# Kernel optimization log

Hardware: AMD Instinct MI355X
Metric: run time of the kernel (lower is better)

Reference implementation:

```python
import jax, jax.numpy as jnp
import numpy as np

H = 4          # number of heads
C = 32         # head dim (H*C == D)
INF = 1e9
EPS = 1e-5


def setup_inputs() -> dict:
    key = jax.random.key(0)
    ks = jax.random.split(key, 8)
    B, N, D = 1, 256, 128
    x = jax.random.normal(ks[0], (B, N, N, D), dtype=jnp.float32)
    mask = jnp.ones((B, N, N), dtype=jnp.float32)
    s = 1.0 / np.sqrt(D)
    return {
        "x": x,
        "mask": mask,
        "ln_w": jnp.ones((D,), jnp.float32),
        "ln_b": jnp.zeros((D,), jnp.float32),
        "w_tri": jax.random.normal(ks[1], (D, H), jnp.float32) * s,
        "w_q": jax.random.normal(ks[2], (D, H * C), jnp.float32) * s,
        "w_k": jax.random.normal(ks[3], (D, H * C), jnp.float32) * s,
        "w_v": jax.random.normal(ks[4], (D, H * C), jnp.float32) * s,
        "w_g": jax.random.normal(ks[5], (D, H * C), jnp.float32) * s,
        "b_g": jnp.ones((H * C,), jnp.float32),
        "w_o": jax.random.normal(ks[6], (H * C, D), jnp.float32) * s,
        "b_o": jnp.zeros((D,), jnp.float32),
    }


def reference(x, mask, ln_w, ln_b, w_tri, w_q, w_k, w_v, w_g, b_g, w_o, b_o):
    B, I, J, D = x.shape
    # LayerNorm over channel dim
    mu = jnp.mean(x, axis=-1, keepdims=True)
    var = jnp.mean(jnp.square(x - mu), axis=-1, keepdims=True)
    xn = (x - mu) * jax.lax.rsqrt(var + EPS) * ln_w + ln_b

    # Triangle bias: linear D->H, permute_final_dims((2,0,1)) -> [B,H,I,J], unsqueeze(-4) -> [B,1,H,I,J]
    tri_bias = jnp.einsum("bijd,dh->bhij", xn, w_tri)[:, None]
    # Mask bias: inf*(mask[...,:,None,None,:]-1) -> [B,I,1,1,J]
    mask_bias = INF * (mask[:, :, None, None, :] - 1.0)

    # Gated MHA per row I, attending across columns J
    q = (xn @ w_q).reshape(B, I, J, H, C) * (1.0 / np.sqrt(C))
    k = (xn @ w_k).reshape(B, I, J, H, C)
    v = (xn @ w_v).reshape(B, I, J, H, C)
    scores = jnp.einsum("bimhc,binhc->bihmn", q, k) + tri_bias + mask_bias
    attn = jax.nn.softmax(scores, axis=-1)
    o = jnp.einsum("bihmn,binhc->bimhc", attn, v)
    g = jax.nn.sigmoid((xn @ w_g + b_g).reshape(B, I, J, H, C))
    o = (g * o).reshape(B, I, J, H * C)
    return o @ w_o + b_o
```

## Files before the change

### kernel.cpp

```cpp
#include <hip/hip_runtime.h>
#include <hip/hip_bf16.h>

#define INF_F 1e9f
#define EPS_F 1e-5f
#define QSCALE 0.1767766952966369f
#define SM_SHIFT 16.0f

typedef __attribute__((ext_vector_type(8))) short short8;
typedef __attribute__((ext_vector_type(4))) float f32x4;

__device__ __forceinline__ unsigned short f2bf(float f) {
    union { float f; unsigned int u; } v; v.f = f;
    unsigned int r = v.u + 0x7FFFu + ((v.u >> 16) & 1u);
    return (unsigned short)(r >> 16);
}
__device__ __forceinline__ float bf2f(unsigned short b) {
    union { unsigned int u; float f; } v; v.u = ((unsigned int)b) << 16; return v.f;
}
__device__ __forceinline__ unsigned int pack2bf(float a, float b) {
    return (unsigned int)f2bf(a) | ((unsigned int)f2bf(b) << 16);
}

__global__ __launch_bounds__(256) void prep_weights(
    const float* __restrict__ wq, const float* __restrict__ wk,
    const float* __restrict__ wv, const float* __restrict__ wg,
    const float* __restrict__ wo, unsigned short* __restrict__ wt)
{
    const int m = blockIdx.x;
    const float* W = (m == 0) ? wq : (m == 1) ? wk : (m == 2) ? wv : (m == 3) ? wg : wo;
    const float scale = (m == 0) ? QSCALE : 1.0f;
    unsigned short* out = wt + m * 16384;
    const int t = threadIdx.x;
    #pragma unroll
    for (int j = 0; j < 8; ++j) {
        int o = t * 64 + j * 8;
        int n = o >> 7, k0 = o & 127;
        short8 v;
        #pragma unroll
        for (int jj = 0; jj < 8; ++jj)
            v[jj] = (short)f2bf(W[(size_t)(k0 + jj) * 128 + n] * scale);
        *reinterpret_cast<short8*>(out + o) = v;
    }
}

__global__ __launch_bounds__(512, 4) void ln_proj_kernel(
    const float* __restrict__ x, const float* __restrict__ ln_w, const float* __restrict__ ln_b,
    const float* __restrict__ w_tri, const unsigned short* __restrict__ wt,
    const float* __restrict__ b_g,
    unsigned short* __restrict__ qb, unsigned short* __restrict__ kb,
    unsigned short* __restrict__ vb, unsigned short* __restrict__ gb,
    float* __restrict__ tri_bias)
{
    __shared__ unsigned short xs[128][136];
    __shared__ unsigned short wb[128][136];
    __shared__ float wt_s[512];
    __shared__ float bgs[128];

    const int tid = threadIdx.x;
    const int p0  = blockIdx.x * 128;

    if (tid < 128) bgs[tid] = b_g[tid];
    wt_s[tid] = w_tri[tid];

    {
        const int c4 = (tid & 31) * 4;
        const float4 lw = *reinterpret_cast<const float4*>(ln_w + c4);
        const float4 lb = *reinterpret_cast<const float4*>(ln_b + c4);
        #pragma unroll
        for (int r = 0; r < 8; ++r) {
            int idx = r * 512 + tid;
            int px  = idx >> 5;
            float4 v = *reinterpret_cast<const float4*>(x + (size_t)(p0 + px) * 128 + c4);
            float s  = v.x + v.y + v.z + v.w;
            float ss = v.x * v.x + v.y * v.y + v.z * v.z + v.w * v.w;
            #pragma unroll
            for (int mk = 1; mk <= 16; mk <<= 1) {
                s  += __shfl_xor(s, mk);
                ss += __shfl_xor(ss, mk);
            }
            float mu   = s * 0.0078125f;
            float rstd = rsqrtf(ss * 0.0078125f - mu * mu + EPS_F);
            float a0 = (v.x - mu) * rstd * lw.x + lb.x;
            float a1 = (v.y - mu) * rstd * lw.y + lb.y;
            float a2 = (v.z - mu) * rstd * lw.z + lb.z;
            float a3 = (v.w - mu) * rstd * lw.w + lb.w;
            *reinterpret_cast<unsigned int*>(&xs[px][c4])     = pack2bf(a0, a1);
            *reinterpret_cast<unsigned int*>(&xs[px][c4 + 2]) = pack2bf(a2, a3);
        }
    }
    __syncthreads();

    {
        const int px = tid >> 2, hh = tid & 3;
        float acc = 0.f;
        #pragma unroll
        for (int kq = 0; kq < 128; kq += 8) {
            short8 xv = *reinterpret_cast<const short8*>(&xs[px][kq]);
            #pragma unroll
            for (int j = 0; j < 8; ++j)
                acc = fmaf(bf2f((unsigned short)xv[j]), wt_s[(kq + j) * 4 + hh], acc);
        }
        tri_bias[hh * 65536 + p0 + px] = acc;
    }

    const int lane = tid & 63, wid = tid >> 6;
    const int lrow = lane & 15, lgrp = lane >> 4;
    const int m0 = (wid >> 1) * 32, n0 = (wid & 1) * 64;

    for (int y = 0; y < 4; ++y) {
        __syncthreads();
        const unsigned short* Wsrc = wt + y * 16384;
        #pragma unroll
        for (int r = 0; r < 4; ++r) {
            int idx = r * 512 + tid;
            int n = idx >> 4, k8 = (idx & 15) * 8;
            *reinterpret_cast<short8*>(&wb[n][k8]) =
                *reinterpret_cast<const short8*>(Wsrc + n * 128 + k8);
        }
        __syncthreads();

        f32x4 acc[2][4];
        #pragma unroll
        for (int mt = 0; mt < 2; ++mt)
            #pragma unroll
            for (int nt = 0; nt < 4; ++nt) acc[mt][nt] = f32x4{0.f, 0.f, 0.f, 0.f};

        #pragma unroll
        for (int kk = 0; kk < 4; ++kk) {
            short8 af[2], bfr[4];
            #pragma unroll
            for (int mt = 0; mt < 2; ++mt)
                af[mt] = *reinterpret_cast<const short8*>(&xs[m0 + mt * 16 + lrow][kk * 32 + lgrp * 8]);
            #pragma unroll
            for (int nt = 0; nt < 4; ++nt)
                bfr[nt] = *reinterpret_cast<const short8*>(&wb[n0 + nt * 16 + lrow][kk * 32 + lgrp * 8]);
            #pragma unroll
            for (int mt = 0; mt < 2; ++mt)
                #pragma unroll
                for (int nt = 0; nt < 4; ++nt)
                    acc[mt][nt] = __builtin_amdgcn_mfma_f32_16x16x32_bf16(af[mt], bfr[nt], acc[mt][nt], 0, 0, 0);
        }
        __syncthreads();

        #pragma unroll
        for (int mt = 0; mt < 2; ++mt)
            #pragma unroll
            for (int nt = 0; nt < 4; ++nt)
                #pragma unroll
                for (int r = 0; r < 4; ++r) {
                    int row = m0 + mt * 16 + lgrp * 4 + r;
                    int col = n0 + nt * 16 + lrow;
                    float v = acc[mt][nt][r];
                    if (y == 3) v = 1.f / (1.f + __expf(-(v + bgs[col])));
                    wb[row][col] = f2bf(v);
                }
        __syncthreads();

        unsigned short* outp = (y == 0) ? qb : (y == 1) ? kb : (y == 2) ? vb : gb;
        #pragma unroll
        for (int r = 0; r < 4; ++r) {
            int idx = r * 512 + tid;
            int px = idx >> 4, c8 = (idx & 15) * 8;
            *reinterpret_cast<short8*>(outp + (size_t)(p0 + px) * 128 + c8) =
                *reinterpret_cast<const short8*>(&wb[px][c8]);
        }
    }
}

__global__ __launch_bounds__(512, 4) void attn_kernel(
    const unsigned short* qbuf, const unsigned short* __restrict__ kbuf,
    const unsigned short* __restrict__ vbuf, const unsigned short* __restrict__ gbuf,
    const float* __restrict__ tri_bias, const float* __restrict__ mask,
    unsigned short* og)
{
    __shared__ unsigned short Ks[256][40];
    __shared__ unsigned short Vt[32][264];
    __shared__ float maskb[256];

    const int tid = threadIdx.x;
    const int i  = blockIdx.x;
    const int h  = blockIdx.y >> 1;
    const int rg = blockIdx.y & 1;
    const size_t base = (size_t)i * 32768 + (size_t)h * 32;

    #pragma unroll
    for (int r = 0; r < 2; ++r) {
        int idx = r * 512 + tid;
        int n = idx >> 2, c8 = (idx & 3) * 8;
        short8 kv = *reinterpret_cast<const short8*>(kbuf + base + (size_t)n * 128 + c8);
        short8 vv = *reinterpret_cast<const short8*>(vbuf + base + (size_t)n * 128 + c8);
        *reinterpret_cast<short8*>(&Ks[n][c8]) = kv;
        #pragma unroll
        for (int j = 0; j < 8; ++j) {
            int row = c8 + j;
            Vt[row][n ^ (((row >> 3) & 3) << 3)] = (unsigned short)vv[j];
        }
    }
    if (tid < 256) maskb[tid] = INF_F * (mask[i * 256 + tid] - 1.0f);
    __syncthreads();

    const int lane = tid & 63;
    const int wid  = tid >> 6;
    const int q    = lane & 15;
    const int g    = lane >> 4;
    const int q0   = rg * 128 + wid * 16;

    short8 qf = *reinterpret_cast<const short8*>(qbuf + base + (size_t)(q0 + q) * 128 + g * 8);

    const float* biasrow = tri_bias + (size_t)h * 65536 + (size_t)(q0 + q) * 256;
    const f32x4 z = {0.f, 0.f, 0.f, 0.f};
    f32x4 oacc[2] = {z, z};
    float lsum = 0.f;
    const int xr0 = (((q >> 3) & 1) << 3);
    const int xr1 = ((((16 + q) >> 3) & 3) << 3);

    #pragma unroll
    for (int ch = 0; ch < 8; ++ch) {
        const int nb = ch * 32;
        short8 kf0 = *reinterpret_cast<const short8*>(&Ks[nb + q][g * 8]);
        short8 kf1 = *reinterpret_cast<const short8*>(&Ks[nb + 16 + q][g * 8]);
        f32x4 s0 = __builtin_amdgcn_mfma_f32_16x16x32_bf16(kf0, qf, z, 0, 0, 0);
        f32x4 s1 = __builtin_amdgcn_mfma_f32_16x16x32_bf16(kf1, qf, z, 0, 0, 0);
        f32x4 bv0 = *reinterpret_cast<const f32x4*>(biasrow + nb + g * 4);
        f32x4 bv1 = *reinterpret_cast<const f32x4*>(biasrow + nb + 16 + g * 4);
        f32x4 mv0 = *reinterpret_cast<const f32x4*>(&maskb[nb + g * 4]);
        f32x4 mv1 = *reinterpret_cast<const f32x4*>(&maskb[nb + 16 + g * 4]);
        s0 += bv0 + mv0;
        s1 += bv1 + mv1;
        float p00 = __expf(s0[0] - SM_SHIFT), p01 = __expf(s0[1] - SM_SHIFT);
        float p02 = __expf(s0[2] - SM_SHIFT), p03 = __expf(s0[3] - SM_SHIFT);
        float p10 = __expf(s1[0] - SM_SHIFT), p11 = __expf(s1[1] - SM_SHIFT);
        float p12 = __expf(s1[2] - SM_SHIFT), p13 = __expf(s1[3] - SM_SHIFT);
        lsum += ((p00 + p01) + (p02 + p03)) + ((p10 + p11) + (p12 + p13));
        unsigned int A0 = pack2bf(p00, p01), A1 = pack2bf(p02, p03);
        unsigned int B0 = pack2bf(p10, p11), B1 = pack2bf(p12, p13);
        unsigned int A16_0 = (unsigned int)__shfl_xor((int)A0, 16);
        unsigned int A16_1 = (unsigned int)__shfl_xor((int)A1, 16);
        unsigned int B16_0 = (unsigned int)__shfl_xor((int)B0, 16);
        unsigned int B16_1 = (unsigned int)__shfl_xor((int)B1, 16);
        unsigned int A32_0 = (unsigned int)__shfl_xor((int)A0, 32);
        unsigned int A32_1 = (unsigned int)__shfl_xor((int)A1, 32);
        unsigned int B32_0 = (unsigned int)__shfl_xor((int)B0, 32);
        unsigned int B32_1 = (unsigned int)__shfl_xor((int)B1, 32);
        unsigned int A48_0 = (unsigned int)__shfl_xor((int)A16_0, 32);
        unsigned int A48_1 = (unsigned int)__shfl_xor((int)A16_1, 32);
        unsigned int B48_0 = (unsigned int)__shfl_xor((int)B16_0, 32);
        unsigned int B48_1 = (unsigned int)__shfl_xor((int)B16_1, 32);
        union { unsigned int u[4]; short8 s; } pu;
        pu.u[0] = (g == 0) ? A0    : (g == 1) ? A48_0 : (g == 2) ? B32_0 : B16_0;
        pu.u[1] = (g == 0) ? A1    : (g == 1) ? A48_1 : (g == 2) ? B32_1 : B16_1;
        pu.u[2] = (g == 0) ? A16_0 : (g == 1) ? A32_0 : (g == 2) ? B48_0 : B0;
        pu.u[3] = (g == 0) ? A16_1 : (g == 1) ? A32_1 : (g == 2) ? B48_1 : B1;
        short8 vf0 = *reinterpret_cast<const short8*>(&Vt[q][(nb + g * 8) ^ xr0]);
        short8 vf1 = *reinterpret_cast<const short8*>(&Vt[16 + q][(nb + g * 8) ^ xr1]);
        oacc[0] = __builtin_amdgcn_mfma_f32_16x16x32_bf16(pu.s, vf0, oacc[0], 0, 0, 0);
        oacc[1] = __builtin_amdgcn_mfma_f32_16x16x32_bf16(pu.s, vf1, oacc[1], 0, 0, 0);
    }

    lsum += __shfl_xor(lsum, 16);
    lsum += __shfl_xor(lsum, 32);

    float linv = 1.0f / lsum;
    #pragma unroll
    for (int r = 0; r < 4; ++r) {
        float li = __shfl(linv, g * 4 + r);
        int m = q0 + g * 4 + r;
        #pragma unroll
        for (int ct = 0; ct < 2; ++ct) {
            int c = ct * 16 + q;
            float gv = bf2f(gbuf[base + (size_t)m * 128 + c]);
            og[base + (size_t)m * 128 + c] = f2bf(oacc[ct][r] * li * gv);
        }
    }
}

__global__ __launch_bounds__(512, 4) void out_proj_kernel(
    const unsigned short* __restrict__ og, const unsigned short* __restrict__ wto,
    const float* __restrict__ b_o, float* __restrict__ out)
{
    __shared__ unsigned short xs[128][136];
    __shared__ unsigned short wb[128][136];
    __shared__ float bos[128];
    const int tid = threadIdx.x;
    const int p0  = blockIdx.x * 128;
    if (tid < 128) bos[tid] = b_o[tid];

    #pragma unroll
    for (int r = 0; r < 4; ++r) {
        int idx = r * 512 + tid;
        int a = idx >> 4, b8 = (idx & 15) * 8;
        *reinterpret_cast<short8*>(&xs[a][b8]) =
            *reinterpret_cast<const short8*>(og + (size_t)(p0 + a) * 128 + b8);
        *reinterpret_cast<short8*>(&wb[a][b8]) =
            *reinterpret_cast<const short8*>(wto + a * 128 + b8);
    }
    __syncthreads();

    const int lane = tid & 63, wid = tid >> 6;
    const int lrow = lane & 15, lgrp = lane >> 4;
    const int m0 = (wid >> 1) * 32, n0 = (wid & 1) * 64;

    f32x4 acc[2][4];
    #pragma unroll
    for (int mt = 0; mt < 2; ++mt)
        #pragma unroll
        for (int nt = 0; nt < 4; ++nt) acc[mt][nt] = f32x4{0.f, 0.f, 0.f, 0.f};

    #pragma unroll
    for (int kk = 0; kk < 4; ++kk) {
        short8 af[2], bfr[4];
        #pragma unroll
        for (int mt = 0; mt < 2; ++mt)
            af[mt] = *reinterpret_cast<const short8*>(&xs[m0 + mt * 16 + lrow][kk * 32 + lgrp * 8]);
        #pragma unroll
        for (int nt = 0; nt < 4; ++nt)
            bfr[nt] = *reinterpret_cast<const short8*>(&wb[n0 + nt * 16 + lrow][kk * 32 + lgrp * 8]);
        #pragma unroll
        for (int mt = 0; mt < 2; ++mt)
            #pragma unroll
            for (int nt = 0; nt < 4; ++nt)
                acc[mt][nt] = __builtin_amdgcn_mfma_f32_16x16x32_bf16(af[mt], bfr[nt], acc[mt][nt], 0, 0, 0);
    }

    #pragma unroll
    for (int mt = 0; mt < 2; ++mt)
        #pragma unroll
        for (int nt = 0; nt < 4; ++nt)
            #pragma unroll
            for (int r = 0; r < 4; ++r) {
                int row = m0 + mt * 16 + lgrp * 4 + r;
                int col = n0 + nt * 16 + lrow;
                out[(size_t)(p0 + row) * 128 + col] = acc[mt][nt][r] + bos[col];
            }
}

extern "C" void kernel_launch(void* const* d_in, const int* in_sizes, int n_in,
                              void* d_out, int out_size, void* d_ws, size_t ws_size,
                              hipStream_t stream)
{
    const float* x     = (const float*)d_in[0];
    const float* mask  = (const float*)d_in[1];
    const float* ln_w  = (const float*)d_in[2];
    const float* ln_b  = (const float*)d_in[3];
    const float* w_tri = (const float*)d_in[4];
    const float* w_q   = (const float*)d_in[5];
    const float* w_k   = (const float*)d_in[6];
    const float* w_v   = (const float*)d_in[7];
    const float* w_g   = (const float*)d_in[8];
    const float* b_g   = (const float*)d_in[9];
    const float* w_o   = (const float*)d_in[10];
    const float* b_o   = (const float*)d_in[11];
    float* out = (float*)d_out;

    unsigned short* qb = (unsigned short*)d_ws;
    unsigned short* kb = qb + 8388608;
    unsigned short* vb = kb + 8388608;
    unsigned short* gb = vb + 8388608;
    float* bias = (float*)(gb + 8388608);
    unsigned short* wt = (unsigned short*)(bias + 4 * 65536);

    prep_weights<<<dim3(5), 256, 0, stream>>>(w_q, w_k, w_v, w_g, w_o, wt);
    ln_proj_kernel<<<512, 512, 0, stream>>>(
        x, ln_w, ln_b, w_tri, wt, b_g, qb, kb, vb, gb, bias);
    attn_kernel<<<dim3(256, 8), 512, 0, stream>>>(
        qb, kb, vb, gb, bias, mask, qb );
    out_proj_kernel<<<512, 512, 0, stream>>>(qb, wt + 4 * 16384, b_o, out);
}
```

Before: 88.23 us.

## Split LN from projection, tile projections per output matrix, use 16x16x16 MFMA for PV

LayerNorm and the triangle bias move into a separate one-wave-per-pixel kernel that writes bf16 normalized activations. The QKVG projection becomes a grid over 64-pixel tiles times four weight matrices, replacing one block that looped over all four. The output projection is retiled the same way. In attention, the shuffle-based repacking of probabilities for the PV MFMA is replaced by 16x16x16 bf16 MFMAs that use the accumulator layout directly, with a new V swizzle. This trades an extra global round trip of normalized activations for more parallelism and fewer shuffles.

```diff
diff --git a/kernel.cpp b/kernel.cpp
--- a/kernel.cpp
+++ b/kernel.cpp
@@ -7,6 +7,7 @@
 #define SM_SHIFT 16.0f
 
 typedef __attribute__((ext_vector_type(8))) short short8;
+typedef __attribute__((ext_vector_type(4))) short bf16x4;
 typedef __attribute__((ext_vector_type(4))) float f32x4;
 
 __device__ __forceinline__ unsigned short f2bf(float f) {
@@ -20,6 +21,20 @@
 __device__ __forceinline__ unsigned int pack2bf(float a, float b) {
     return (unsigned int)f2bf(a) | ((unsigned int)f2bf(b) << 16);
 }
+
+#if defined(__has_builtin)
+#if __has_builtin(__builtin_amdgcn_mfma_f32_16x16x16bf16_1k)
+#define MFMA16BF(a, b, c) __builtin_amdgcn_mfma_f32_16x16x16bf16_1k(a, b, c, 0, 0, 0)
+#endif
+#endif
+#ifndef MFMA16BF
+__device__ __forceinline__ f32x4 mfma16bf_asm(bf16x4 a, bf16x4 b, f32x4 c) {
+    asm volatile("v_mfma_f32_16x16x16_bf16 %0, %1, %2, %0\n\ts_nop 7\n\ts_nop 7"
+                 : "+v"(c) : "v"(a), "v"(b));
+    return c;
+}
+#define MFMA16BF(a, b, c) mfma16bf_asm(a, b, c)
+#endif
 
 __global__ __launch_bounds__(256) void prep_weights(
     const float* __restrict__ wq, const float* __restrict__ wk,
@@ -43,127 +58,115 @@
     }
 }
 
-__global__ __launch_bounds__(512, 4) void ln_proj_kernel(
+__global__ __launch_bounds__(256) void ln_kernel(
     const float* __restrict__ x, const float* __restrict__ ln_w, const float* __restrict__ ln_b,
-    const float* __restrict__ w_tri, const unsigned short* __restrict__ wt,
+    const float* __restrict__ w_tri, unsigned short* __restrict__ xnb,
+    float* __restrict__ tri_bias)
+{
+    const int lane = threadIdx.x & 63;
+    const int wv   = threadIdx.x >> 6;
+    const int px   = blockIdx.x * 4 + wv;
+
+    const float2 v = *reinterpret_cast<const float2*>(x + (size_t)px * 128 + lane * 2);
+    float s = v.x + v.y, ss = v.x * v.x + v.y * v.y;
+    #pragma unroll
+    for (int m = 1; m <= 32; m <<= 1) { s += __shfl_xor(s, m); ss += __shfl_xor(ss, m); }
+    float mu   = s * 0.0078125f;
+    float rstd = rsqrtf(ss * 0.0078125f - mu * mu + EPS_F);
+    const float2 lw = *reinterpret_cast<const float2*>(ln_w + lane * 2);
+    const float2 lb = *reinterpret_cast<const float2*>(ln_b + lane * 2);
+    float a0 = (v.x - mu) * rstd * lw.x + lb.x;
+    float a1 = (v.y - mu) * rstd * lw.y + lb.y;
+    *reinterpret_cast<unsigned int*>(xnb + (size_t)px * 128 + lane * 2) = pack2bf(a0, a1);
+
+    f32x4 wa = *reinterpret_cast<const f32x4*>(w_tri + lane * 8);
+    f32x4 wb = *reinterpret_cast<const f32x4*>(w_tri + lane * 8 + 4);
+    f32x4 ph;
+    #pragma unroll
+    for (int j = 0; j < 4; ++j) ph[j] = a0 * wa[j] + a1 * wb[j];
+    #pragma unroll
+    for (int m = 1; m <= 32; m <<= 1) {
+        #pragma unroll
+        for (int j = 0; j < 4; ++j) ph[j] += __shfl_xor(ph[j], m);
+    }
+    if (lane < 4) {
+        float pv = (lane == 0) ? ph[0] : (lane == 1) ? ph[1] : (lane == 2) ? ph[2] : ph[3];
+        tri_bias[lane * 65536 + px] = pv;
+    }
+}
+
+__global__ __launch_bounds__(256) void proj_kernel(
+    const unsigned short* __restrict__ xnb, const unsigned short* __restrict__ wt,
     const float* __restrict__ b_g,
     unsigned short* __restrict__ qb, unsigned short* __restrict__ kb,
-    unsigned short* __restrict__ vb, unsigned short* __restrict__ gb,
-    float* __restrict__ tri_bias)
-{
-    __shared__ unsigned short xs[128][136];
-    __shared__ unsigned short wb[128][136];
-    __shared__ float wt_s[512];
+    unsigned short* __restrict__ vb, unsigned short* __restrict__ gb)
+{
+    __shared__ unsigned short As[64][136];
+    __shared__ unsigned short Bs[128][136];
     __shared__ float bgs[128];
 
     const int tid = threadIdx.x;
-    const int p0  = blockIdx.x * 128;
-
+    const int p0  = blockIdx.x * 64;
+    const int y   = blockIdx.y;
     if (tid < 128) bgs[tid] = b_g[tid];
-    wt_s[tid] = w_tri[tid];
-
-    {
-        const int c4 = (tid & 31) * 4;
-        const float4 lw = *reinterpret_cast<const float4*>(ln_w + c4);
-        const float4 lb = *reinterpret_cast<const float4*>(ln_b + c4);
-        #pragma unroll
-        for (int r = 0; r < 8; ++r) {
-            int idx = r * 512 + tid;
-            int px  = idx >> 5;
-            float4 v = *reinterpret_cast<const float4*>(x + (size_t)(p0 + px) * 128 + c4);
-            float s  = v.x + v.y + v.z + v.w;
-            float ss = v.x * v.x + v.y * v.y + v.z * v.z + v.w * v.w;
-            #pragma unroll
-            for (int mk = 1; mk <= 16; mk <<= 1) {
-                s  += __shfl_xor(s, mk);
-                ss += __shfl_xor(ss, mk);
-            }
-            float mu   = s * 0.0078125f;
-            float rstd = rsqrtf(ss * 0.0078125f - mu * mu + EPS_F);
-            float a0 = (v.x - mu) * rstd * lw.x + lb.x;
-            float a1 = (v.y - mu) * rstd * lw.y + lb.y;
-            float a2 = (v.z - mu) * rstd * lw.z + lb.z;
-            float a3 = (v.w - mu) * rstd * lw.w + lb.w;
-            *reinterpret_cast<unsigned int*>(&xs[px][c4])     = pack2bf(a0, a1);
-            *reinterpret_cast<unsigned int*>(&xs[px][c4 + 2]) = pack2bf(a2, a3);
-        }
-    }
-    __syncthreads();
-
-    {
-        const int px = tid >> 2, hh = tid & 3;
-        float acc = 0.f;
-        #pragma unroll
-        for (int kq = 0; kq < 128; kq += 8) {
-            short8 xv = *reinterpret_cast<const short8*>(&xs[px][kq]);
-            #pragma unroll
-            for (int j = 0; j < 8; ++j)
-                acc = fmaf(bf2f((unsigned short)xv[j]), wt_s[(kq + j) * 4 + hh], acc);
-        }
-        tri_bias[hh * 65536 + p0 + px] = acc;
-    }
+
+    #pragma unroll
+    for (int r = 0; r < 4; ++r) {
+        int idx = r * 256 + tid;
+        int px = idx >> 4, k8 = (idx & 15) * 8;
+        *reinterpret_cast<short8*>(&As[px][k8]) =
+            *reinterpret_cast<const short8*>(xnb + (size_t)(p0 + px) * 128 + k8);
+    }
+    const unsigned short* W = wt + y * 16384;
+    #pragma unroll
+    for (int r = 0; r < 8; ++r) {
+        int idx = r * 256 + tid;
+        int n = idx >> 4, k8 = (idx & 15) * 8;
+        *reinterpret_cast<short8*>(&Bs[n][k8]) =
+            *reinterpret_cast<const short8*>(W + n * 128 + k8);
+    }
+    __syncthreads();
 
     const int lane = tid & 63, wid = tid >> 6;
     const int lrow = lane & 15, lgrp = lane >> 4;
-    const int m0 = (wid >> 1) * 32, n0 = (wid & 1) * 64;
-
-    for (int y = 0; y < 4; ++y) {
-        __syncthreads();
-        const unsigned short* Wsrc = wt + y * 16384;
+    const int m0 = wid * 16;
+
+    f32x4 acc[8];
+    #pragma unroll
+    for (int nt = 0; nt < 8; ++nt) acc[nt] = f32x4{0.f, 0.f, 0.f, 0.f};
+
+    #pragma unroll
+    for (int kk = 0; kk < 4; ++kk) {
+        short8 af = *reinterpret_cast<const short8*>(&As[m0 + lrow][kk * 32 + lgrp * 8]);
+        short8 bfr[8];
+        #pragma unroll
+        for (int nt = 0; nt < 8; ++nt)
+            bfr[nt] = *reinterpret_cast<const short8*>(&Bs[nt * 16 + lrow][kk * 32 + lgrp * 8]);
+        #pragma unroll
+        for (int nt = 0; nt < 8; ++nt)
+            acc[nt] = __builtin_amdgcn_mfma_f32_16x16x32_bf16(af, bfr[nt], acc[nt], 0, 0, 0);
+    }
+    __syncthreads();
+
+    #pragma unroll
+    for (int nt = 0; nt < 8; ++nt)
         #pragma unroll
         for (int r = 0; r < 4; ++r) {
-            int idx = r * 512 + tid;
-            int n = idx >> 4, k8 = (idx & 15) * 8;
-            *reinterpret_cast<short8*>(&wb[n][k8]) =
-                *reinterpret_cast<const short8*>(Wsrc + n * 128 + k8);
+            int row = m0 + lgrp * 4 + r;
+            int col = nt * 16 + lrow;
+            float vv = acc[nt][r];
+            if (y == 3) vv = 1.f / (1.f + __expf(-(vv + bgs[col])));
+            As[row][col] = f2bf(vv);
         }
-        __syncthreads();
-
-        f32x4 acc[2][4];
-        #pragma unroll
-        for (int mt = 0; mt < 2; ++mt)
-            #pragma unroll
-            for (int nt = 0; nt < 4; ++nt) acc[mt][nt] = f32x4{0.f, 0.f, 0.f, 0.f};
-
-        #pragma unroll
-        for (int kk = 0; kk < 4; ++kk) {
-            short8 af[2], bfr[4];
-            #pragma unroll
-            for (int mt = 0; mt < 2; ++mt)
-                af[mt] = *reinterpret_cast<const short8*>(&xs[m0 + mt * 16 + lrow][kk * 32 + lgrp * 8]);
-            #pragma unroll
-            for (int nt = 0; nt < 4; ++nt)
-                bfr[nt] = *reinterpret_cast<const short8*>(&wb[n0 + nt * 16 + lrow][kk * 32 + lgrp * 8]);
-            #pragma unroll
-            for (int mt = 0; mt < 2; ++mt)
-                #pragma unroll
-                for (int nt = 0; nt < 4; ++nt)
-                    acc[mt][nt] = __builtin_amdgcn_mfma_f32_16x16x32_bf16(af[mt], bfr[nt], acc[mt][nt], 0, 0, 0);
-        }
-        __syncthreads();
-
-        #pragma unroll
-        for (int mt = 0; mt < 2; ++mt)
-            #pragma unroll
-            for (int nt = 0; nt < 4; ++nt)
-                #pragma unroll
-                for (int r = 0; r < 4; ++r) {
-                    int row = m0 + mt * 16 + lgrp * 4 + r;
-                    int col = n0 + nt * 16 + lrow;
-                    float v = acc[mt][nt][r];
-                    if (y == 3) v = 1.f / (1.f + __expf(-(v + bgs[col])));
-                    wb[row][col] = f2bf(v);
-                }
-        __syncthreads();
-
-        unsigned short* outp = (y == 0) ? qb : (y == 1) ? kb : (y == 2) ? vb : gb;
-        #pragma unroll
-        for (int r = 0; r < 4; ++r) {
-            int idx = r * 512 + tid;
-            int px = idx >> 4, c8 = (idx & 15) * 8;
-            *reinterpret_cast<short8*>(outp + (size_t)(p0 + px) * 128 + c8) =
-                *reinterpret_cast<const short8*>(&wb[px][c8]);
-        }
+    __syncthreads();
+
+    unsigned short* outp = (y == 0) ? qb : (y == 1) ? kb : (y == 2) ? vb : gb;
+    #pragma unroll
+    for (int r = 0; r < 4; ++r) {
+        int idx = r * 256 + tid;
+        int px = idx >> 4, c8 = (idx & 15) * 8;
+        *reinterpret_cast<short8*>(outp + (size_t)(p0 + px) * 128 + c8) =
+            *reinterpret_cast<const short8*>(&As[px][c8]);
     }
 }
 
@@ -193,7 +196,7 @@
         #pragma unroll
         for (int j = 0; j < 8; ++j) {
             int row = c8 + j;
-            Vt[row][n ^ (((row >> 3) & 3) << 3)] = (unsigned short)vv[j];
+            Vt[row][n ^ (((row >> 3) & 3) << 4)] = (unsigned short)vv[j];
         }
     }
     if (tid < 256) maskb[tid] = INF_F * (mask[i * 256 + tid] - 1.0f);
@@ -211,8 +214,8 @@
     const f32x4 z = {0.f, 0.f, 0.f, 0.f};
     f32x4 oacc[2] = {z, z};
     float lsum = 0.f;
-    const int xr0 = (((q >> 3) & 1) << 3);
-    const int xr1 = ((((16 + q) >> 3) & 3) << 3);
+    const int xr0 = ((q >> 3) & 1) << 4;
+    const int xr1 = ((2 + (q >> 3)) & 3) << 4;
 
     #pragma unroll
     for (int ch = 0; ch < 8; ++ch) {
@@ -232,29 +235,17 @@
         float p10 = __expf(s1[0] - SM_SHIFT), p11 = __expf(s1[1] - SM_SHIFT);
         float p12 = __expf(s1[2] - SM_SHIFT), p13 = __expf(s1[3] - SM_SHIFT);
         lsum += ((p00 + p01) + (p02 + p03)) + ((p10 + p11) + (p12 + p13));
-        unsigned int A0 = pack2bf(p00, p01), A1 = pack2bf(p02, p03);
-        unsigned int B0 = pack2bf(p10, p11), B1 = pack2bf(p12, p13);
-        unsigned int A16_0 = (unsigned int)__shfl_xor((int)A0, 16);
-        unsigned int A16_1 = (unsigned int)__shfl_xor((int)A1, 16);
-        unsigned int B16_0 = (unsigned int)__shfl_xor((int)B0, 16);
-        unsigned int B16_1 = (unsigned int)__shfl_xor((int)B1, 16);
-        unsigned int A32_0 = (unsigned int)__shfl_xor((int)A0, 32);
-        unsigned int A32_1 = (unsigned int)__shfl_xor((int)A1, 32);
-        unsigned int B32_0 = (unsigned int)__shfl_xor((int)B0, 32);
-        unsigned int B32_1 = (unsigned int)__shfl_xor((int)B1, 32);
-        unsigned int A48_0 = (unsigned int)__shfl_xor((int)A16_0, 32);
-        unsigned int A48_1 = (unsigned int)__shfl_xor((int)A16_1, 32);
-        unsigned int B48_0 = (unsigned int)__shfl_xor((int)B16_0, 32);
-        unsigned int B48_1 = (unsigned int)__shfl_xor((int)B16_1, 32);
-        union { unsigned int u[4]; short8 s; } pu;
-        pu.u[0] = (g == 0) ? A0    : (g == 1) ? A48_0 : (g == 2) ? B32_0 : B16_0;
-        pu.u[1] = (g == 0) ? A1    : (g == 1) ? A48_1 : (g == 2) ? B32_1 : B16_1;
-        pu.u[2] = (g == 0) ? A16_0 : (g == 1) ? A32_0 : (g == 2) ? B48_0 : B0;
-        pu.u[3] = (g == 0) ? A16_1 : (g == 1) ? A32_1 : (g == 2) ? B48_1 : B1;
-        short8 vf0 = *reinterpret_cast<const short8*>(&Vt[q][(nb + g * 8) ^ xr0]);
-        short8 vf1 = *reinterpret_cast<const short8*>(&Vt[16 + q][(nb + g * 8) ^ xr1]);
-        oacc[0] = __builtin_amdgcn_mfma_f32_16x16x32_bf16(pu.s, vf0, oacc[0], 0, 0, 0);
-        oacc[1] = __builtin_amdgcn_mfma_f32_16x16x32_bf16(pu.s, vf1, oacc[1], 0, 0, 0);
+        union { unsigned int u[2]; bf16x4 s; } pA, pB;
+        pA.u[0] = pack2bf(p00, p01); pA.u[1] = pack2bf(p02, p03);
+        pB.u[0] = pack2bf(p10, p11); pB.u[1] = pack2bf(p12, p13);
+        bf16x4 vA0 = *reinterpret_cast<const bf16x4*>(&Vt[q][(nb + g * 4) ^ xr0]);
+        bf16x4 vA1 = *reinterpret_cast<const bf16x4*>(&Vt[16 + q][(nb + g * 4) ^ xr1]);
+        bf16x4 vB0 = *reinterpret_cast<const bf16x4*>(&Vt[q][(nb + 16 + g * 4) ^ xr0]);
+        bf16x4 vB1 = *reinterpret_cast<const bf16x4*>(&Vt[16 + q][(nb + 16 + g * 4) ^ xr1]);
+        oacc[0] = MFMA16BF(pA.s, vA0, oacc[0]);
+        oacc[1] = MFMA16BF(pA.s, vA1, oacc[1]);
+        oacc[0] = MFMA16BF(pB.s, vB0, oacc[0]);
+        oacc[1] = MFMA16BF(pB.s, vB1, oacc[1]);
     }
 
     lsum += __shfl_xor(lsum, 16);
@@ -274,64 +265,62 @@
     }
 }
 
-__global__ __launch_bounds__(512, 4) void out_proj_kernel(
+__global__ __launch_bounds__(256) void out_proj_kernel(
     const unsigned short* __restrict__ og, const unsigned short* __restrict__ wto,
     const float* __restrict__ b_o, float* __restrict__ out)
 {
-    __shared__ unsigned short xs[128][136];
-    __shared__ unsigned short wb[128][136];
+    __shared__ unsigned short As[64][136];
+    __shared__ unsigned short Bs[128][136];
     __shared__ float bos[128];
+
     const int tid = threadIdx.x;
-    const int p0  = blockIdx.x * 128;
+    const int p0  = blockIdx.x * 64;
     if (tid < 128) bos[tid] = b_o[tid];
 
     #pragma unroll
     for (int r = 0; r < 4; ++r) {
-        int idx = r * 512 + tid;
-        int a = idx >> 4, b8 = (idx & 15) * 8;
-        *reinterpret_cast<short8*>(&xs[a][b8]) =
-            *reinterpret_cast<const short8*>(og + (size_t)(p0 + a) * 128 + b8);
-        *reinterpret_cast<short8*>(&wb[a][b8]) =
-            *reinterpret_cast<const short8*>(wto + a * 128 + b8);
+        int idx = r * 256 + tid;
+        int px = idx >> 4, k8 = (idx & 15) * 8;
+        *reinterpret_cast<short8*>(&As[px][k8]) =
+            *reinterpret_cast<const short8*>(og + (size_t)(p0 + px) * 128 + k8);
+    }
+    #pragma unroll
+    for (int r = 0; r < 8; ++r) {
+        int idx = r * 256 + tid;
+        int n = idx >> 4, k8 = (idx & 15) * 8;
+        *reinterpret_cast<short8*>(&Bs[n][k8]) =
+            *reinterpret_cast<const short8*>(wto + n * 128 + k8);
     }
     __syncthreads();
 
     const int lane = tid & 63, wid = tid >> 6;
     const int lrow = lane & 15, lgrp = lane >> 4;
-    const int m0 = (wid >> 1) * 32, n0 = (wid & 1) * 64;
-
-    f32x4 acc[2][4];
-    #pragma unroll
-    for (int mt = 0; mt < 2; ++mt)
-        #pragma unroll
-        for (int nt = 0; nt < 4; ++nt) acc[mt][nt] = f32x4{0.f, 0.f, 0.f, 0.f};
+    const int m0 = wid * 16;
+
+    f32x4 acc[8];
+    #pragma unroll
+    for (int nt = 0; nt < 8; ++nt) acc[nt] = f32x4{0.f, 0.f, 0.f, 0.f};
 
     #pragma unroll
     for (int kk = 0; kk < 4; ++kk) {
-        short8 af[2], bfr[4];
-        #pragma unroll
-        for (int mt = 0; mt < 2; ++mt)
-            af[mt] = *reinterpret_cast<const short8*>(&xs[m0 + mt * 16 + lrow][kk * 32 + lgrp * 8]);
-        #pragma unroll
-        for (int nt = 0; nt < 4; ++nt)
-            bfr[nt] = *reinterpret_cast<const short8*>(&wb[n0 + nt * 16 + lrow][kk * 32 + lgrp * 8]);
-        #pragma unroll
-        for (int mt = 0; mt < 2; ++mt)
-            #pragma unroll
-            for (int nt = 0; nt < 4; ++nt)
-                acc[mt][nt] = __builtin_amdgcn_mfma_f32_16x16x32_bf16(af[mt], bfr[nt], acc[mt][nt], 0, 0, 0);
-    }
-
-    #pragma unroll
-    for (int mt = 0; mt < 2; ++mt)
-        #pragma unroll
-        for (int nt = 0; nt < 4; ++nt)
-            #pragma unroll
-            for (int r = 0; r < 4; ++r) {
-                int row = m0 + mt * 16 + lgrp * 4 + r;
-                int col = n0 + nt * 16 + lrow;
-                out[(size_t)(p0 + row) * 128 + col] = acc[mt][nt][r] + bos[col];
-            }
+        short8 af = *reinterpret_cast<const short8*>(&As[m0 + lrow][kk * 32 + lgrp * 8]);
+        short8 bfr[8];
+        #pragma unroll
+        for (int nt = 0; nt < 8; ++nt)
+            bfr[nt] = *reinterpret_cast<const short8*>(&Bs[nt * 16 + lrow][kk * 32 + lgrp * 8]);
+        #pragma unroll
+        for (int nt = 0; nt < 8; ++nt)
+            acc[nt] = __builtin_amdgcn_mfma_f32_16x16x32_bf16(af, bfr[nt], acc[nt], 0, 0, 0);
+    }
+
+    #pragma unroll
+    for (int nt = 0; nt < 8; ++nt)
+        #pragma unroll
+        for (int r = 0; r < 4; ++r) {
+            int row = m0 + lgrp * 4 + r;
+            int col = nt * 16 + lrow;
+            out[(size_t)(p0 + row) * 128 + col] = acc[nt][r] + bos[col];
+        }
 }
 
 extern "C" void kernel_launch(void* const* d_in, const int* in_sizes, int n_in,
@@ -358,11 +347,12 @@
     unsigned short* gb = vb + 8388608;
     float* bias = (float*)(gb + 8388608);
     unsigned short* wt = (unsigned short*)(bias + 4 * 65536);
-
+    unsigned short* xnb = wt + 5 * 16384;
+
+    ln_kernel<<<16384, 256, 0, stream>>>(x, ln_w, ln_b, w_tri, xnb, bias);
     prep_weights<<<dim3(5), 256, 0, stream>>>(w_q, w_k, w_v, w_g, w_o, wt);
-    ln_proj_kernel<<<512, 512, 0, stream>>>(
-        x, ln_w, ln_b, w_tri, wt, b_g, qb, kb, vb, gb, bias);
+    proj_kernel<<<dim3(1024, 4), 256, 0, stream>>>(xnb, wt, b_g, qb, kb, vb, gb);
     attn_kernel<<<dim3(256, 8), 512, 0, stream>>>(
         qb, kb, vb, gb, bias, mask, qb );
-    out_proj_kernel<<<512, 512, 0, stream>>>(qb, wt + 4 * 16384, b_o, out);
-}
+    out_proj_kernel<<<1024, 256, 0, stream>>>(qb, wt + 4 * 16384, b_o, out);
+}
```

New measurement: 116.8 us. 1.32x slower.
